# Kernel optimization log

Measured on AMD Instinct MI355X. Metric: run time of the kernel, lower is better.

## Reference

```python
import jax, jax.numpy as jnp
import numpy as np
import math

HIDDEN = 2048
HEADS = 16
HEAD_DIM = HIDDEN // HEADS
MAX_SEQ = 4096
ROPE_BASE = 10000.0


def rope_cos_sin(seq_len):
    # (seq_len, head_dim//2) angle table
    inv_freq = 1.0 / (ROPE_BASE ** (jnp.arange(0, HEAD_DIM, 2, dtype=jnp.float32) / HEAD_DIM))
    t = jnp.arange(seq_len, dtype=jnp.float32)
    ang = jnp.einsum('s,f->sf', t, inv_freq)
    return jnp.cos(ang), jnp.sin(ang)


def apply_rope(x, cos, sin):
    # x: (b, s, h, d); interleaved complex pairs along last dim
    b, s, h, d = x.shape
    xr = x.reshape(b, s, h, d // 2, 2)
    x0, x1 = xr[..., 0], xr[..., 1]
    c = cos[:s][None, :, None, :]
    sn = sin[:s][None, :, None, :]
    o0 = x0 * c - x1 * sn
    o1 = x0 * sn + x1 * c
    return jnp.stack([o0, o1], axis=-1).reshape(b, s, h, d)


def setup_inputs() -> dict:
    key = jax.random.key(0)
    k1, k2, k3, k4, k5, k6 = jax.random.split(key, 6)
    B, SQ, SK = 2, 2048, 2048
    x = jax.random.normal(k1, (B, SQ, HIDDEN), dtype=jnp.float32)
    enc = jax.random.normal(k2, (B, SK, HIDDEN), dtype=jnp.float32)
    mask = jnp.ones((B, SK), dtype=jnp.int32)
    scale = 0.02
    Wq = jax.random.normal(k3, (HIDDEN, HIDDEN), dtype=jnp.float32) * scale
    Wk = jax.random.normal(k4, (HIDDEN, HIDDEN), dtype=jnp.float32) * scale
    Wv = jax.random.normal(k5, (HIDDEN, HIDDEN), dtype=jnp.float32) * scale
    Wo = jax.random.normal(k6, (HIDDEN, HIDDEN), dtype=jnp.float32) * scale
    return {"x": x, "encoder_output": enc, "encoder_attention_mask": mask,
            "Wq": Wq, "Wk": Wk, "Wv": Wv, "Wo": Wo}


def reference(x, encoder_output, encoder_attention_mask, Wq, Wk, Wv, Wo):
    B, SQ, _ = x.shape
    SK = encoder_output.shape[1]
    # nn.Linear(bias=False): y = x @ W^T
    q = (x @ Wq.T).reshape(B, SQ, HEADS, HEAD_DIM)
    k = (encoder_output @ Wk.T).reshape(B, SK, HEADS, HEAD_DIM)
    v = (encoder_output @ Wv.T).reshape(B, SK, HEADS, HEAD_DIM)
    cos, sin = rope_cos_sin(max(SQ, SK))
    q = apply_rope(q, cos, sin)
    k = apply_rope(k, cos, sin)
    scale = math.sqrt(HEAD_DIM)
    # (b, h, sq, sk) scores
    scores = jnp.einsum('bqhd,bkhd->bhqk', q, k) / scale
    mask = encoder_attention_mask[:, None, None, :]
    scores = jnp.where(mask == 0, -jnp.inf, scores)
    attn = jax.nn.softmax(scores, axis=-1)
    out = jnp.einsum('bhqk,bkhd->bqhd', attn, v).reshape(B, SQ, HIDDEN)
    return out @ Wo.T
```

## Files before the change

kernel.cpp:

```cpp
#include <hip/hip_runtime.h>
#include <stdint.h>


#define LOG2E 1.44269504088896340736f
#define INV2PI 0.15915494309189535f

typedef __attribute__((ext_vector_type(8))) short bf16x8;
typedef __attribute__((ext_vector_type(8))) uint16_t u16x8;
typedef __attribute__((ext_vector_type(4))) uint16_t u16x4;
typedef __attribute__((ext_vector_type(4))) float f32x4;

__device__ __forceinline__ uint16_t f2bf(float f) {
  union { float f; uint32_t i; } v; v.f = f;
  uint32_t x = v.i;
  return (uint16_t)((x + 0x7fffu + ((x >> 16) & 1u)) >> 16);
}
__device__ __forceinline__ uint32_t f_as_u(float f) { union { float f; uint32_t u; } v; v.f = f; return v.u; }
__device__ __forceinline__ float u_as_f(uint32_t u) { union { uint32_t u; float f; } v; v.u = u; return v.f; }
__device__ __forceinline__ void glds16(const void* g, void* l) {
  __builtin_amdgcn_global_load_lds((const __attribute__((address_space(1))) void*)g,
                                   (__attribute__((address_space(3))) void*)l, 16, 0, 0);
}

__global__ __launch_bounds__(256) void convert_xe(const float* __restrict__ x,
                                                  const float* __restrict__ enc,
                                                  uint16_t* __restrict__ xb,
                                                  uint16_t* __restrict__ encb) {
  const int blk = blockIdx.x;
  const float* src = (blk < 4096) ? x : enc;
  uint16_t* dst = (blk < 4096) ? xb : encb;
  const long off = ((long)(blk & 4095) * 256 + threadIdx.x) * 8;
  const f32x4 a = *(const f32x4*)(src + off);
  const f32x4 b = *(const f32x4*)(src + off + 4);
  u16x8 o;
#pragma unroll
  for (int j = 0; j < 4; ++j) { o[j] = f2bf(a[j]); o[4 + j] = f2bf(b[j]); }
  *(u16x8*)(dst + off) = o;
}

__global__ __launch_bounds__(256) void convert_w4(const float* __restrict__ Wq,
                                                  const float* __restrict__ Wk,
                                                  const float* __restrict__ Wv,
                                                  const float* __restrict__ Wo,
                                                  uint16_t* __restrict__ W4) {
  const int blk = blockIdx.x;
  const int sec = blk >> 11;
  const long off = ((long)(blk & 2047) * 256 + threadIdx.x) * 8;
  const float* src = (sec == 0) ? Wq : (sec == 1) ? Wk : (sec == 2) ? Wv : Wo;
  const f32x4 a = *(const f32x4*)(src + off);
  const f32x4 b = *(const f32x4*)(src + off + 4);
  u16x8 o;
#pragma unroll
  for (int j = 0; j < 4; ++j) { o[j] = f2bf(a[j]); o[4 + j] = f2bf(b[j]); }
  *(u16x8*)(W4 + (long)sec * 4194304 + off) = o;
}

__global__ __launch_bounds__(256) void mask_bias(const int* __restrict__ m,
                                                 float* __restrict__ bias) {
  const int i = blockIdx.x * 256 + threadIdx.x;
  bias[i] = m[i] ? 0.0f : -__builtin_inff();
}

__device__ __forceinline__ void epi_rope_store(uint16_t* C, const f32x4& a, int rowbase,
                                               int c, float oscale) {
  const int f = (c >> 1) & 63;
  const float inv = __builtin_amdgcn_exp2f((float)f * (-13.287712379549449f / 64.0f));
  const float sgn = (c & 1) ? 1.0f : -1.0f;
#pragma unroll
  for (int r = 0; r < 4; ++r) {
    const float val = a[r];
    const float partner = __shfl_xor(val, 1);
    const int s = (rowbase + r) & 2047;
    const float rev = __builtin_amdgcn_fractf((float)s * inv * INV2PI);
    const float sn = __builtin_amdgcn_sinf(rev);
    const float cs = __builtin_amdgcn_cosf(rev);
    C[(long)(rowbase + r) * 2048 + c] = f2bf((val * cs + sgn * partner * sn) * oscale);
  }
}

__global__ __launch_bounds__(512, 2) void gemm256(const uint16_t* __restrict__ A0,
                                                  const uint16_t* __restrict__ A1,
                                                  const uint16_t* __restrict__ W,
                                                  uint16_t* __restrict__ Qb,
                                                  uint16_t* __restrict__ Kb,
                                                  uint16_t* __restrict__ Vtb,
                                                  int M, int N, int K, float oscale) {
  __shared__ __align__(16) uint16_t As[2][2][8192];
  __shared__ __align__(16) uint16_t Bs[2][2][8192];
  const int tid = threadIdx.x;
  const int lane = tid & 63;
  const int w = tid >> 6;
  const int r16 = lane & 15, quad = lane >> 4;
  const int wm = w >> 2, wn = w & 3;

  const int nby = M >> 8;
  const int nwg = gridDim.x;
  const int wg = ((int)blockIdx.x & 7) * (nwg >> 3) + ((int)blockIdx.x >> 3);
  const int by = wg % nby, bx = wg / nby;
  const int m0 = by << 8, n0 = bx << 8;

  const uint16_t* A = (n0 >= 2048) ? A1 : A0;

  const int srow = 2 * w * 16 + (lane >> 2);
  const int ssl = (lane & 3) ^ ((srow >> 1) & 3);
  const uint16_t* Ag0 = A + (long)(m0 + srow) * K + ssl * 8;
  const uint16_t* Ag1 = Ag0 + (long)16 * K;
  const uint16_t* Bg0 = W + (long)(n0 + srow) * K + ssl * 8;
  const uint16_t* Bg1 = Bg0 + (long)16 * K;
  const int ldso = w << 10;

  const int sw = (r16 >> 1) & 3;
  const int aoff = (wm * 128 + r16) * 32 + ((quad ^ sw) << 3);
  const int boff = (wn * 64 + r16) * 32 + ((quad ^ sw) << 3);

  f32x4 acc[8][4] = {};
  bf16x8 af[4], bfr[4];

#define SCHED0() __builtin_amdgcn_sched_barrier(0)
#define G_STAGE_A(BUF, KK, T) do { \
    glds16(Ag0 + (long)(T) * 64 + (KK) * 32, &As[BUF][KK][ldso]); \
    glds16(Ag1 + (long)(T) * 64 + (KK) * 32, &As[BUF][KK][ldso + 512]); } while (0)
#define G_STAGE_B(BUF, KK, T) do { \
    glds16(Bg0 + (long)(T) * 64 + (KK) * 32, &Bs[BUF][KK][ldso]); \
    glds16(Bg1 + (long)(T) * 64 + (KK) * 32, &Bs[BUF][KK][ldso + 512]); } while (0)
#define LDS_B(BUF, KK) do { _Pragma("unroll") \
    for (int i = 0; i < 4; ++i) bfr[i] = *(const bf16x8*)&Bs[BUF][KK][boff + i * 512]; } while (0)
#define LDS_A(BUF, KK, MH) do { _Pragma("unroll") \
    for (int i = 0; i < 4; ++i) af[i] = *(const bf16x8*)&As[BUF][KK][aoff + ((MH) * 4 + i) * 512]; } while (0)
#define MFMA16(MH) do { __builtin_amdgcn_s_setprio(1); _Pragma("unroll") \
    for (int mi = 0; mi < 4; ++mi) { _Pragma("unroll") \
      for (int nt = 0; nt < 4; ++nt) \
        acc[(MH) * 4 + mi][nt] = __builtin_amdgcn_mfma_f32_16x16x32_bf16(af[mi], bfr[nt], acc[(MH) * 4 + mi][nt], 0, 0, 0); } \
    __builtin_amdgcn_s_setprio(0); } while (0)
#define VMBAR(NN) do { SCHED0(); \
    asm volatile("s_waitcnt vmcnt(" #NN ")" ::: "memory"); \
    __builtin_amdgcn_s_barrier(); \
    SCHED0(); } while (0)
#define TILE_ITER(T, BC, BN) do { \
    G_STAGE_A(BN, 0, (T) + 1); LDS_B(BC, 0); LDS_A(BC, 0, 0); MFMA16(0); \
    G_STAGE_B(BN, 0, (T) + 1); LDS_A(BC, 0, 1); MFMA16(1); \
    VMBAR(4); \
    G_STAGE_A(BN, 1, (T) + 1); LDS_B(BC, 1); LDS_A(BC, 1, 0); MFMA16(0); \
    G_STAGE_B(BN, 1, (T) + 1); LDS_A(BC, 1, 1); MFMA16(1); \
    VMBAR(4); } while (0)

  G_STAGE_A(0, 0, 0); G_STAGE_B(0, 0, 0); G_STAGE_A(0, 1, 0); G_STAGE_B(0, 1, 0);
  VMBAR(4);

  const int NT = K >> 6;
  int t = 0;
  for (; t + 2 < NT; t += 2) { TILE_ITER(t, 0, 1); TILE_ITER(t + 1, 1, 0); }
  TILE_ITER(t, 0, 1);

  LDS_B(1, 0); LDS_A(1, 0, 0); MFMA16(0);
  LDS_A(1, 0, 1); MFMA16(1);
  VMBAR(0);
  LDS_B(1, 1); LDS_A(1, 1, 0); MFMA16(0);
  LDS_A(1, 1, 1); MFMA16(1);

#undef G_STAGE_A
#undef G_STAGE_B
#undef LDS_A
#undef LDS_B
#undef TILE_ITER

#pragma unroll
  for (int mt = 0; mt < 8; ++mt)
#pragma unroll
    for (int nt = 0; nt < 4; ++nt) {
      const int col = n0 + wn * 64 + nt * 16 + r16;
      const int rowbase = m0 + wm * 128 + mt * 16 + quad * 4;
      if (n0 < 2048) {
        epi_rope_store(Qb, acc[mt][nt], rowbase, col, oscale);
      } else if (n0 < 4096) {
        epi_rope_store(Kb, acc[mt][nt], rowbase, col - 2048, 1.0f);
      } else {
        const int c = col - 4096;
        const int h = c >> 7, d = c & 127;
        const int b = rowbase >> 11, s = rowbase & 2047;
        u16x4 pk;
#pragma unroll
        for (int r = 0; r < 4; ++r) pk[r] = f2bf(acc[mt][nt][r]);
        *(u16x4*)(Vtb + (long)((b * 16 + h) * 128 + d) * 2048 + s) = pk;
      }
    }
}

__global__ __launch_bounds__(512, 2) void gemm_proj(const uint16_t* __restrict__ A0,
                                                    const uint16_t* __restrict__ W,
                                                    float* __restrict__ C,
                                                    int M, int N, int K) {
  __shared__ __align__(16) uint16_t As[2][2][4096];
  __shared__ __align__(16) uint16_t Bs[2][2][8192];
  const int tid = threadIdx.x;
  const int lane = tid & 63;
  const int w = tid >> 6;
  const int r16 = lane & 15, quad = lane >> 4;
  const int wm = w >> 2, wn = w & 3;

  const int nby = M >> 7;
  const int nwg = gridDim.x;
  const int wg = ((int)blockIdx.x & 7) * (nwg >> 3) + ((int)blockIdx.x >> 3);
  const int by = wg % nby, bx = wg / nby;
  const int m0 = by << 7, n0 = bx << 8;

  const int sa_row = 16 * w + (lane >> 2);
  const int sb_row = 32 * w + (lane >> 2);
  const int ssl = (lane & 3) ^ (((lane >> 2) >> 1) & 3);
  const uint16_t* Ag = A0 + (long)(m0 + sa_row) * K + ssl * 8;
  const uint16_t* Bg0 = W + (long)(n0 + sb_row) * K + ssl * 8;
  const uint16_t* Bg1 = Bg0 + (long)16 * K;

  const int sw = (r16 >> 1) & 3;
  const int aoff = (wm * 64 + r16) * 32 + ((quad ^ sw) << 3);
  const int boff = (wn * 64 + r16) * 32 + ((quad ^ sw) << 3);

  f32x4 acc[4][4] = {};
  bf16x8 af[4], bfr[4];

#define SCHED0() __builtin_amdgcn_sched_barrier(0)
#define VMBAR(NN) do { SCHED0(); \
    asm volatile("s_waitcnt vmcnt(" #NN ")" ::: "memory"); \
    __builtin_amdgcn_s_barrier(); \
    SCHED0(); } while (0)
#define PG_STAGE_A(BUF, KK, T) \
    glds16(Ag + (long)(T) * 64 + (KK) * 32, &As[BUF][KK][w * 512])
#define PG_STAGE_B(BUF, KK, T) do { \
    glds16(Bg0 + (long)(T) * 64 + (KK) * 32, &Bs[BUF][KK][2 * w * 512]); \
    glds16(Bg1 + (long)(T) * 64 + (KK) * 32, &Bs[BUF][KK][2 * w * 512 + 512]); } while (0)
#define PLDS_B(BUF, KK) do { _Pragma("unroll") \
    for (int i = 0; i < 4; ++i) bfr[i] = *(const bf16x8*)&Bs[BUF][KK][boff + i * 512]; } while (0)
#define PLDS_A(BUF, KK) do { _Pragma("unroll") \
    for (int i = 0; i < 4; ++i) af[i] = *(const bf16x8*)&As[BUF][KK][aoff + i * 512]; } while (0)
#define PMFMA(MT0, MT1) do { __builtin_amdgcn_s_setprio(1); _Pragma("unroll") \
    for (int mi = (MT0); mi < (MT1); ++mi) { _Pragma("unroll") \
      for (int nt = 0; nt < 4; ++nt) \
        acc[mi][nt] = __builtin_amdgcn_mfma_f32_16x16x32_bf16(af[mi], bfr[nt], acc[mi][nt], 0, 0, 0); } \
    __builtin_amdgcn_s_setprio(0); } while (0)
#define PTILE(T, BC, BN) do { \
    PG_STAGE_A(BN, 0, (T) + 1); PLDS_B(BC, 0); PLDS_A(BC, 0); PMFMA(0, 2); \
    PG_STAGE_B(BN, 0, (T) + 1); PMFMA(2, 4); \
    VMBAR(3); \
    PG_STAGE_A(BN, 1, (T) + 1); PLDS_B(BC, 1); PLDS_A(BC, 1); PMFMA(0, 2); \
    PG_STAGE_B(BN, 1, (T) + 1); PMFMA(2, 4); \
    VMBAR(3); } while (0)

  PG_STAGE_A(0, 0, 0); PG_STAGE_B(0, 0, 0); PG_STAGE_A(0, 1, 0); PG_STAGE_B(0, 1, 0);
  VMBAR(3);

  const int NT = K >> 6;
  int t = 0;
  for (; t + 2 < NT; t += 2) { PTILE(t, 0, 1); PTILE(t + 1, 1, 0); }
  PTILE(t, 0, 1);

  PLDS_B(1, 0); PLDS_A(1, 0); PMFMA(0, 4);
  VMBAR(0);
  PLDS_B(1, 1); PLDS_A(1, 1); PMFMA(0, 4);

#undef PG_STAGE_A
#undef PG_STAGE_B
#undef PLDS_A
#undef PLDS_B
#undef PMFMA
#undef PTILE
#undef VMBAR
#undef SCHED0

#pragma unroll
  for (int mt = 0; mt < 4; ++mt)
#pragma unroll
    for (int nt = 0; nt < 4; ++nt) {
      const int col = n0 + wn * 64 + nt * 16 + r16;
      const int rowbase = m0 + wm * 64 + mt * 16 + quad * 4;
#pragma unroll
      for (int r = 0; r < 4; ++r)
        C[(long)(rowbase + r) * N + col] = acc[mt][nt][r];
    }
}

__global__ __launch_bounds__(512, 4) void attn_kernel(const uint16_t* __restrict__ Q,
                                                      const uint16_t* __restrict__ K,
                                                      const uint16_t* __restrict__ Vt,
                                                      const float* __restrict__ bias,
                                                      uint16_t* __restrict__ O) {
  __shared__ __align__(16) uint16_t Ks[2][32 * 128];
  __shared__ __align__(16) uint16_t Vts[2][128 * 32];
  __shared__ __align__(16) uint16_t Ps[8][16 * 40];
  const int tid = threadIdx.x;
  const int lane = tid & 63;
  const int w = tid >> 6;
  const int r16 = lane & 15, quad = lane >> 4;
  const int h = blockIdx.y, b = blockIdx.z;
  const int qbase = blockIdx.x * 128 + w * 16;

  bf16x8 qf[4];
  {
    const uint16_t* qb = Q + ((long)(b * 2048 + qbase + r16)) * 2048 + h * 128 + quad * 8;
#pragma unroll
    for (int c = 0; c < 4; ++c) qf[c] = *(const bf16x8*)(qb + c * 32);
  }
  f32x4 oacc[8] = {};
  float li[4] = {};

  uint16_t* PsW = &Ps[w][0];
  const float* brow = bias + b * 2048;

  const int kkey = 4 * w + quad;
  const uint16_t* kg = K + ((long)(b * 2048 + kkey)) * 2048 + h * 128
                         + 8 * (r16 ^ (kkey & 7));
  const int vdim = 16 * w + (lane >> 2);
  const uint16_t* vg = Vt + ((long)((b * 16 + h) * 128 + vdim)) * 2048
                          + 8 * ((lane & 3) ^ ((lane >> 2) & 3));

  glds16(kg, &Ks[0][w * 512]);
  glds16(vg, &Vts[0][w * 512]);
  kg += 32 * 2048;
  vg += 32;
  float bn0 = brow[r16], bn1 = brow[16 + r16];

  auto body = [&](int k0, const uint16_t* Kc, const uint16_t* Vc,
                  uint16_t* Kn, uint16_t* Vn, bool pf) {
    __syncthreads();
    const float bc0 = bn0, bc1 = bn1;
    if (pf) {
      glds16(kg, Kn + w * 512);
      glds16(vg, Vn + w * 512);
      kg += 32 * 2048;
      vg += 32;
      bn0 = brow[k0 + 32 + r16];
      bn1 = brow[k0 + 48 + r16];
    }
#pragma unroll
    for (int ct = 0; ct < 2; ++ct) {
      const int key = ct * 16 + r16;
      const int kb = key & 7;
      bf16x8 kf[4];
#pragma unroll
      for (int c = 0; c < 4; ++c)
        kf[c] = *(const bf16x8*)(Kc + key * 128 + ((4 * c + quad) ^ kb) * 8);
      const float bv = ct ? bc1 : bc0;
      const int pc = ct * 2 + (r16 >> 3);
      f32x4 s = {};
#pragma unroll
      for (int c = 0; c < 4; ++c)
        s = __builtin_amdgcn_mfma_f32_16x16x32_bf16(qf[c], kf[c], s, 0, 0, 0);
#pragma unroll
      for (int r = 0; r < 4; ++r) {
        const float p = __builtin_amdgcn_exp2f(s[r] + bv);
        const uint32_t pb = f_as_u(p) + 0x8000u;
        const int row = quad * 4 + r;
        PsW[row * 40 + ((pc ^ quad) << 3) + (r16 & 7)] = (uint16_t)(pb >> 16);
        li[r] += u_as_f(pb & 0xffff0000u);
      }
    }
    bf16x8 pa = *(const bf16x8*)(PsW + r16 * 40 + ((quad ^ (r16 >> 2)) << 3));
#pragma unroll
    for (int nt = 0; nt < 8; ++nt) {
      const int dim = nt * 16 + r16;
      bf16x8 vf = *(const bf16x8*)(Vc + dim * 32 + ((quad ^ (dim & 3)) << 3));
      oacc[nt] = __builtin_amdgcn_mfma_f32_16x16x32_bf16(pa, vf, oacc[nt], 0, 0, 0);
    }
  };

  for (int kt2 = 0; kt2 < 32; ++kt2) {
    body(64 * kt2,      &Ks[0][0], &Vts[0][0], &Ks[1][0], &Vts[1][0], true);
    body(64 * kt2 + 32, &Ks[1][0], &Vts[1][0], &Ks[0][0], &Vts[0][0], kt2 < 31);
  }

#pragma unroll
  for (int off = 1; off < 16; off <<= 1)
#pragma unroll
    for (int r = 0; r < 4; ++r) li[r] += __shfl_xor(li[r], off);

  uint16_t* ob = O + ((long)(b * 2048 + qbase)) * 2048 + h * 128;
  float inv_l[4];
#pragma unroll
  for (int r = 0; r < 4; ++r) inv_l[r] = 1.0f / li[r];
#pragma unroll
  for (int nt = 0; nt < 8; ++nt)
#pragma unroll
    for (int r = 0; r < 4; ++r)
      ob[(long)(quad * 4 + r) * 2048 + nt * 16 + r16] = f2bf(oacc[nt][r] * inv_l[r]);
}

extern "C" void kernel_launch(void* const* d_in, const int* in_sizes, int n_in,
                              void* d_out, int out_size, void* d_ws, size_t ws_size,
                              hipStream_t stream) {
  const float* x   = (const float*)d_in[0];
  const float* enc = (const float*)d_in[1];
  const int*   msk = (const int*)d_in[2];
  const float* Wq  = (const float*)d_in[3];
  const float* Wk  = (const float*)d_in[4];
  const float* Wv  = (const float*)d_in[5];
  const float* Wo  = (const float*)d_in[6];
  float* out = (float*)d_out;

  const long NELT = 8L * 1024 * 1024;
  const long WELT = 4L * 1024 * 1024;
  uint16_t* Qb  = (uint16_t*)d_ws;
  uint16_t* Kb  = Qb + NELT;
  uint16_t* Vtb = Kb + NELT;
  uint16_t* W4  = Vtb + NELT;
  float* biasb  = (float*)(W4 + 4 * WELT);
  uint16_t* xb   = (uint16_t*)d_out;
  uint16_t* encb = xb + NELT;
  uint16_t* Ob   = W4;

  const float cs_exp = 0.088388347648318447f * LOG2E;

  convert_xe<<<8192, 256, 0, stream>>>(x, enc, xb, encb);
  convert_w4<<<8192, 256, 0, stream>>>(Wq, Wk, Wv, Wo, W4);
  mask_bias<<<16, 256, 0, stream>>>(msk, biasb);

  gemm256<<<384, 512, 0, stream>>>(xb, encb, W4, Qb, Kb, Vtb,
                                   4096, 6144, 2048, cs_exp);

  attn_kernel<<<dim3(16, 16, 2), 512, 0, stream>>>(Qb, Kb, Vtb, biasb, Ob);

  gemm_proj<<<256, 512, 0, stream>>>(Ob, W4 + 3 * WELT, out, 4096, 2048, 2048);
}
```

Before: 447.7 us.

## Replace output projection GEMM with simpler 128x128-tile double-buffered kernel

Swaps the hand-pipelined 128x256-tile, 512-thread output projection GEMM for a 256-thread kernel with 128x128 tiles on a 2D grid. The new kernel double-buffers 32-wide K slices through LDS and uses plain __syncthreads instead of explicit vmcnt waits and scheduling barriers. It also drops the XCD-aware block remapping and the LDS swizzle. The aim is more workgroups to spread across CUs, in exchange for less data reuse per tile, more barriers, and possible LDS bank conflicts.

```diff
diff --git a/kernel.cpp b/kernel.cpp
--- a/kernel.cpp
+++ b/kernel.cpp
@@ -162,7 +162,10 @@
 #undef G_STAGE_B
 #undef LDS_A
 #undef LDS_B
+#undef MFMA16
 #undef TILE_ITER
+#undef VMBAR
+#undef SCHED0
 
 #pragma unroll
   for (int mt = 0; mt < 8; ++mt)
@@ -186,92 +189,65 @@
     }
 }
 
-__global__ __launch_bounds__(512, 2) void gemm_proj(const uint16_t* __restrict__ A0,
+__global__ __launch_bounds__(256) void gemm_proj128(const uint16_t* __restrict__ A,
                                                     const uint16_t* __restrict__ W,
                                                     float* __restrict__ C,
                                                     int M, int N, int K) {
-  __shared__ __align__(16) uint16_t As[2][2][4096];
-  __shared__ __align__(16) uint16_t Bs[2][2][8192];
+  __shared__ __align__(16) uint16_t As[2][128 * 32];
+  __shared__ __align__(16) uint16_t Bs[2][128 * 32];
   const int tid = threadIdx.x;
   const int lane = tid & 63;
   const int w = tid >> 6;
   const int r16 = lane & 15, quad = lane >> 4;
-  const int wm = w >> 2, wn = w & 3;
-
-  const int nby = M >> 7;
-  const int nwg = gridDim.x;
-  const int wg = ((int)blockIdx.x & 7) * (nwg >> 3) + ((int)blockIdx.x >> 3);
-  const int by = wg % nby, bx = wg / nby;
-  const int m0 = by << 7, n0 = bx << 8;
-
-  const int sa_row = 16 * w + (lane >> 2);
-  const int sb_row = 32 * w + (lane >> 2);
-  const int ssl = (lane & 3) ^ (((lane >> 2) >> 1) & 3);
-  const uint16_t* Ag = A0 + (long)(m0 + sa_row) * K + ssl * 8;
-  const uint16_t* Bg0 = W + (long)(n0 + sb_row) * K + ssl * 8;
-  const uint16_t* Bg1 = Bg0 + (long)16 * K;
-
-  const int sw = (r16 >> 1) & 3;
-  const int aoff = (wm * 64 + r16) * 32 + ((quad ^ sw) << 3);
-  const int boff = (wn * 64 + r16) * 32 + ((quad ^ sw) << 3);
-
+  const int m0 = blockIdx.y * 128, n0 = blockIdx.x * 128;
+  const int wm = (w >> 1) * 64, wn = (w & 1) * 64;
   f32x4 acc[4][4] = {};
-  bf16x8 af[4], bfr[4];
-
-#define SCHED0() __builtin_amdgcn_sched_barrier(0)
-#define VMBAR(NN) do { SCHED0(); \
-    asm volatile("s_waitcnt vmcnt(" #NN ")" ::: "memory"); \
-    __builtin_amdgcn_s_barrier(); \
-    SCHED0(); } while (0)
-#define PG_STAGE_A(BUF, KK, T) \
-    glds16(Ag + (long)(T) * 64 + (KK) * 32, &As[BUF][KK][w * 512])
-#define PG_STAGE_B(BUF, KK, T) do { \
-    glds16(Bg0 + (long)(T) * 64 + (KK) * 32, &Bs[BUF][KK][2 * w * 512]); \
-    glds16(Bg1 + (long)(T) * 64 + (KK) * 32, &Bs[BUF][KK][2 * w * 512 + 512]); } while (0)
-#define PLDS_B(BUF, KK) do { _Pragma("unroll") \
-    for (int i = 0; i < 4; ++i) bfr[i] = *(const bf16x8*)&Bs[BUF][KK][boff + i * 512]; } while (0)
-#define PLDS_A(BUF, KK) do { _Pragma("unroll") \
-    for (int i = 0; i < 4; ++i) af[i] = *(const bf16x8*)&As[BUF][KK][aoff + i * 512]; } while (0)
-#define PMFMA(MT0, MT1) do { __builtin_amdgcn_s_setprio(1); _Pragma("unroll") \
-    for (int mi = (MT0); mi < (MT1); ++mi) { _Pragma("unroll") \
-      for (int nt = 0; nt < 4; ++nt) \
-        acc[mi][nt] = __builtin_amdgcn_mfma_f32_16x16x32_bf16(af[mi], bfr[nt], acc[mi][nt], 0, 0, 0); } \
-    __builtin_amdgcn_s_setprio(0); } while (0)
-#define PTILE(T, BC, BN) do { \
-    PG_STAGE_A(BN, 0, (T) + 1); PLDS_B(BC, 0); PLDS_A(BC, 0); PMFMA(0, 2); \
-    PG_STAGE_B(BN, 0, (T) + 1); PMFMA(2, 4); \
-    VMBAR(3); \
-    PG_STAGE_A(BN, 1, (T) + 1); PLDS_B(BC, 1); PLDS_A(BC, 1); PMFMA(0, 2); \
-    PG_STAGE_B(BN, 1, (T) + 1); PMFMA(2, 4); \
-    VMBAR(3); } while (0)
-
-  PG_STAGE_A(0, 0, 0); PG_STAGE_B(0, 0, 0); PG_STAGE_A(0, 1, 0); PG_STAGE_B(0, 1, 0);
-  VMBAR(3);
-
-  const int NT = K >> 6;
-  int t = 0;
-  for (; t + 2 < NT; t += 2) { PTILE(t, 0, 1); PTILE(t + 1, 1, 0); }
-  PTILE(t, 0, 1);
-
-  PLDS_B(1, 0); PLDS_A(1, 0); PMFMA(0, 4);
-  VMBAR(0);
-  PLDS_B(1, 1); PLDS_A(1, 1); PMFMA(0, 4);
-
-#undef PG_STAGE_A
-#undef PG_STAGE_B
-#undef PLDS_A
-#undef PLDS_B
-#undef PMFMA
-#undef PTILE
-#undef VMBAR
-#undef SCHED0
+  const int srow = 32 * w + (lane >> 2);
+  const int scol = (lane & 3) * 8;
+  const uint16_t* Ag = A + (long)(m0 + srow) * K + scol;
+  const uint16_t* Wg = W + (long)(n0 + srow) * K + scol;
+  const int co = 2 * w * 512;
+
+  glds16(Ag, &As[0][co]);
+  glds16(Ag + (long)16 * K, &As[0][co + 512]);
+  glds16(Wg, &Bs[0][co]);
+  glds16(Wg + (long)16 * K, &Bs[0][co + 512]);
+
+  auto body = [&](int k1, const uint16_t* Ac, const uint16_t* Bc,
+                  uint16_t* An, uint16_t* Bn, bool pf) {
+    __syncthreads();
+    if (pf) {
+      glds16(Ag + k1, An + co);
+      glds16(Ag + k1 + (long)16 * K, An + co + 512);
+      glds16(Wg + k1, Bn + co);
+      glds16(Wg + k1 + (long)16 * K, Bn + co + 512);
+    }
+    bf16x8 af[4], bfr[4];
+#pragma unroll
+    for (int mt = 0; mt < 4; ++mt)
+      af[mt] = *(const bf16x8*)(Ac + (wm + mt * 16 + r16) * 32 + quad * 8);
+#pragma unroll
+    for (int nt = 0; nt < 4; ++nt)
+      bfr[nt] = *(const bf16x8*)(Bc + (wn + nt * 16 + r16) * 32 + quad * 8);
+#pragma unroll
+    for (int mt = 0; mt < 4; ++mt)
+#pragma unroll
+      for (int nt = 0; nt < 4; ++nt)
+        acc[mt][nt] = __builtin_amdgcn_mfma_f32_16x16x32_bf16(af[mt], bfr[nt], acc[mt][nt], 0, 0, 0);
+  };
+
+  const int NK2 = K >> 6;
+  for (int kk = 0; kk < NK2; ++kk) {
+    body((2 * kk + 1) * 32, &As[0][0], &Bs[0][0], &As[1][0], &Bs[1][0], true);
+    body((2 * kk + 2) * 32, &As[1][0], &Bs[1][0], &As[0][0], &Bs[0][0], kk < NK2 - 1);
+  }
 
 #pragma unroll
   for (int mt = 0; mt < 4; ++mt)
 #pragma unroll
     for (int nt = 0; nt < 4; ++nt) {
-      const int col = n0 + wn * 64 + nt * 16 + r16;
-      const int rowbase = m0 + wm * 64 + mt * 16 + quad * 4;
+      const int col = n0 + wn + nt * 16 + r16;
+      const int rowbase = m0 + wm + mt * 16 + quad * 4;
 #pragma unroll
       for (int r = 0; r < 4; ++r)
         C[(long)(rowbase + r) * N + col] = acc[mt][nt][r];
@@ -417,5 +393,6 @@
 
   attn_kernel<<<dim3(16, 16, 2), 512, 0, stream>>>(Qb, Kb, Vtb, biasb, Ob);
 
-  gemm_proj<<<256, 512, 0, stream>>>(Ob, W4 + 3 * WELT, out, 4096, 2048, 2048);
-}
+  gemm_proj128<<<dim3(16, 32), 256, 0, stream>>>(Ob, W4 + 3 * WELT, out,
+                                                 4096, 2048, 2048);
+}
```

Result: no change. 449.1 us (+0.3%).
